# Kernel tuning notes

Measured on AMD Instinct MI355X. Metric: run time of the kernel, lower is better.

The kernel has to match this reference:

```python
import jax, jax.numpy as jnp
import numpy as np

B, S, E, H = 4, 1024, 768, 12
DH = E // H  # per-head dim = 64
PRIOR_VAR = 0.01


def _kl(mu, logvar):
    # kl_regularizer from the source: logvar (units,) broadcasts against mu (in,units)
    t = (jnp.log(PRIOR_VAR) - 1.0 - logvar
         + jnp.log1p(jnp.exp(logvar)) / PRIOR_VAR
         + mu * mu / PRIOR_VAR)
    return 0.5 * jnp.mean(t)


def _linear_first(x, w_mu, w_sigma):
    mu = x @ w_mu
    W_Sigma = jnp.log1p(jnp.exp(w_sigma))            # softplus(w_sigma)
    xs = x / x.shape[-1]                              # x / dim (dim = last dim of x)
    xx = jnp.sum(xs * xs, axis=-1, keepdims=True)     # [B,S,1]
    Sigma = jax.nn.softplus(xx * W_Sigma)             # [B,S,E]
    return mu, Sigma, _kl(w_mu, w_sigma)


def _linear_not_first(mu_in, Sigma_in, w_mu, w_sigma):
    mu = mu_in @ w_mu
    W_Sigma = jnp.log1p(jnp.exp(w_sigma))
    wm = w_mu / jnp.sqrt(jnp.float32(w_mu.shape[0]))  # w_mu / sqrt(in_dim)
    S1 = Sigma_in @ (wm * wm)                         # w^T Sigma_in w
    xs = mu_in / mu_in.shape[-1]
    S2 = jnp.sum(xs * xs, axis=-1, keepdims=True) * W_Sigma
    S3 = jnp.sum(Sigma_in, axis=-1, keepdims=True) * W_Sigma / W_Sigma.shape[-1]
    Sigma = jax.nn.softplus(S1 + S2 + S3)
    return mu, Sigma, _kl(w_mu, w_sigma)


def _heads(x):
    # [B,S,E] -> [B,H,S,DH]
    return x.reshape(B, S, H, DH).transpose(0, 2, 1, 3)


def setup_inputs() -> dict:
    key = jax.random.key(0)
    ks = jax.random.split(key, 9)
    glorot = lambda k: jax.random.normal(k, (E, E), jnp.float32) * jnp.sqrt(2.0 / (E + E))
    sig = lambda k: jax.random.uniform(k, (E,), jnp.float32, minval=-4.6, maxval=-2.25)
    return {
        "x": jax.random.normal(ks[0], (B, S, E), jnp.float32),
        "wq_mu": glorot(ks[1]), "wq_sigma": sig(ks[2]),
        "wk_mu": glorot(ks[3]), "wk_sigma": sig(ks[4]),
        "wv_mu": glorot(ks[5]), "wv_sigma": sig(ks[6]),
        "wo_mu": glorot(ks[7]), "wo_sigma": sig(ks[8]),
    }


def reference(x, wq_mu, wq_sigma, wk_mu, wk_sigma, wv_mu, wv_sigma, wo_mu, wo_sigma):
    # dropout is identity in eval mode (training=False)
    mq, sq, klq = _linear_first(x, wq_mu, wq_sigma)
    mk, sk, klk = _linear_first(x, wk_mu, wk_sigma)
    mv, sv, klv = _linear_first(x, wv_mu, wv_sigma)
    mq, sq, mk, sk, mv, sv = map(_heads, (mq, sq, mk, sk, mv, sv))

    dk = jnp.float32(DH)
    mu_score = jnp.einsum('bhqd,bhkd->bhqk', mq, mk)
    a = jnp.einsum('bhqd,bhkd->bhqk', mq * mq / dk, sk)
    b = jnp.einsum('bhqd,bhkd->bhqk', mk * mk / dk, sq)   # matmul(mk^2/dk, sq^T) as in TF source
    c = jnp.einsum('bhqd,bhkd->bhqk', sq / jnp.sqrt(dk), sk / jnp.sqrt(dk))
    sigma_score = a + b + c

    mu_scaled = mu_score / jnp.sqrt(dk)
    sigma_scaled = sigma_score / dk
    w = jax.nn.softmax(mu_scaled, axis=-1)               # [B,H,S,S]
    wd = jnp.float32(S)
    grad = (w - w * w) ** 2
    Sw = grad * sigma_scaled / wd

    mu_att = jnp.einsum('bhqk,bhkd->bhqd', w, mv)
    d = jnp.einsum('bhqk,bhkd->bhqd', w * w / wd, sv)
    e = jnp.einsum('bhqk,bhkd->bhqd', Sw, mv * mv / wd)
    f = jnp.einsum('bhqk,bhkd->bhqd', Sw / jnp.sqrt(wd), sv / jnp.sqrt(wd))
    sig_att = jax.nn.softplus(d + e + f)

    mu_cat = mu_att.transpose(0, 2, 1, 3).reshape(B, S, E)
    sig_cat = sig_att.transpose(0, 2, 1, 3).reshape(B, S, E)

    mu_out, Sigma_out, klo = _linear_not_first(mu_cat, sig_cat, wo_mu, wo_sigma)
    Sigma_out = jax.nn.softplus(Sigma_out)               # extra softplus in call()
    kl = klq + klk + klv + klo
    return mu_out, Sigma_out, kl
```

## Files before the change

### kernel.cpp

```cpp
#include <hip/hip_runtime.h>
#include <math.h>

#define EN 768
#define SN 1024
#define HN 12
#define BSN 4096
#define BSE 3145728

typedef __attribute__((ext_vector_type(8))) short bf16x8;
typedef __attribute__((ext_vector_type(4))) float f32x4;
typedef __attribute__((ext_vector_type(4))) unsigned short u16x4;
typedef unsigned short u16;

#define OFF_XX   0u
#define OFF_RC   16384u
#define OFF_WSIG 32768u
#define OFF_KL   45056u
#define OFF_ZI   49152u
#define OFF_WT   262144u
#define OFF_QH   4980736u
#define OFF_KH   11272192u
#define OFF_SQD  17563648u
#define OFF_SKD  23855104u
#define OFF_MVT  30146560u
#define OFF_MV2  36438016u
#define OFF_SVT  42729472u
#define OFF_MUH  49020928u
#define OFF_SGH  55312384u

__device__ __forceinline__ float sp_f(float x){
  return fmaxf(x, 0.f) + log1pf(__expf(-fabsf(x)));
}
__device__ __forceinline__ u16 f2b(float f){
  unsigned u = __float_as_uint(f);
  return (u16)((u + 0x7fffu + ((u>>16)&1u)) >> 16);
}
__device__ __forceinline__ float b2f(u16 h){
  return __uint_as_float(((unsigned)h)<<16);
}
__device__ __forceinline__ f32x4 mfma16(bf16x8 a, bf16x8 b, f32x4 c){
  return __builtin_amdgcn_mfma_f32_16x16x32_bf16(a, b, c, 0, 0, 0);
}
__device__ __forceinline__ bf16x8 ldsr(const u16* t, int row, int sg){
  int a16 = (row<<3) + (sg ^ (row&7));
  return *(const bf16x8*)(t + (a16<<3));
}
__device__ __forceinline__ void stage64(u16* dst, const u16* src, int rstride, int tid){
  #pragma unroll
  for (int it=0; it<2; ++it){
    int idx = (it<<8) + tid;
    int row = idx>>3, seg = idx&7;
    bf16x8 v = *(const bf16x8*)(src + (long)row*rstride + (seg<<3));
    int a16 = (row<<3) + (seg ^ (row&7));
    *(bf16x8*)(dst + (a16<<3)) = v;
  }
}

__device__ __forceinline__ float blk_reduce(float v, float* tmp){
  #pragma unroll
  for (int off = 32; off; off >>= 1) v += __shfl_down(v, off, 64);
  int w = threadIdx.x >> 6;
  if ((threadIdx.x & 63) == 0) tmp[w] = v;
  __syncthreads();
  float r = 0.f;
  if (threadIdx.x == 0) r = tmp[0] + tmp[1] + tmp[2] + tmp[3];
  __syncthreads();
  return r;
}

__global__ void k_prep(const float* __restrict__ s0, const float* __restrict__ s1,
                       const float* __restrict__ s2, const float* __restrict__ s3,
                       float* __restrict__ wsig, float* __restrict__ klacc){
  __shared__ float tmp[4];
  const float* src = (blockIdx.x==0)?s0:(blockIdx.x==1)?s1:(blockIdx.x==2)?s2:s3;
  int l = blockIdx.x;
  float ssum=0.f, spsum=0.f;
  for (int j=threadIdx.x; j<EN; j+=256){
    float sg = src[j];
    float w  = log1pf(__expf(sg));
    wsig[l*EN+j] = w;
    ssum += sg; spsum += w;
  }
  float a = blk_reduce(ssum, tmp);
  float b = blk_reduce(spsum, tmp);
  if (threadIdx.x==0){ atomicAdd(&klacc[1], a); atomicAdd(&klacc[2], b); }
}

__global__ void k_xx(const float* __restrict__ x, float* __restrict__ xx){
  __shared__ float tmp[4];
  int r = blockIdx.x;
  const float* xr = x + (long)r*EN;
  float s=0.f;
  for (int j=threadIdx.x; j<EN; j+=256){ float v = xr[j]; s += v*v; }
  float t = blk_reduce(s, tmp);
  if (threadIdx.x==0) xx[r] = t*(1.0f/589824.0f);
}

__global__ void k_mu2(const float* __restrict__ w0, const float* __restrict__ w1,
                      const float* __restrict__ w2, const float* __restrict__ w3,
                      float* __restrict__ klacc){
  __shared__ float tmp[4];
  const float* w = (blockIdx.y==0)?w0:(blockIdx.y==1)?w1:(blockIdx.y==2)?w2:w3;
  const float4* w4 = (const float4*)w;
  float s=0.f;
  for (int i=blockIdx.x*256+threadIdx.x; i<147456; i+=gridDim.x*256){
    float4 v = w4[i];
    s += v.x*v.x + v.y*v.y + v.z*v.z + v.w*v.w;
  }
  float r = blk_reduce(s, tmp);
  if (threadIdx.x==0) atomicAdd(&klacc[0], r);
}

__global__ void k_wt(const float* __restrict__ w0, const float* __restrict__ w1,
                     const float* __restrict__ w2, const float* __restrict__ w3,
                     u16* __restrict__ wt){
  __shared__ float t[64*65];
  const float* W = (blockIdx.z==0)?w0:(blockIdx.z==1)?w1:(blockIdx.z==2)?w2:w3;
  u16* WT = wt + (long)blockIdx.z*589824;
  int r0 = blockIdx.y<<6, c0 = blockIdx.x<<6;
  int tid = threadIdx.x;
  #pragma unroll
  for (int it=0; it<16; ++it){
    int idx=(it<<8)+tid; int r=idx>>6, c=idx&63;
    t[c*65+r] = W[(long)(r0+r)*EN + c0+c];
  }
  __syncthreads();
  #pragma unroll
  for (int it=0; it<16; ++it){
    int idx=(it<<8)+tid; int c=idx>>6, r=idx&63;
    WT[(long)(c0+c)*EN + r0+r] = f2b(t[c*65+r]);
  }
}

__global__ void k_sigarr(const float* __restrict__ xx, const float* __restrict__ wsig,
                         u16* __restrict__ sqd, u16* __restrict__ skd){
  int r = blockIdx.x;
  float xr = xx[r];
  for (int c=threadIdx.x; c<EN; c+=256){
    sqd[(long)r*EN+c] = f2b(sp_f(xr*wsig[c])*(1.0f/64.0f));
    skd[(long)r*EN+c] = f2b(sp_f(xr*wsig[EN+c])*(1.0f/64.0f));
  }
}

__global__ void k_svt(const float* __restrict__ xx, const float* __restrict__ wsig,
                      u16* __restrict__ svT){
  __shared__ float sxx[64], swv[64];
  int kt=blockIdx.x, h=blockIdx.y, b=blockIdx.z, tid=threadIdx.x;
  if (tid < 64){
    sxx[tid] = xx[(long)b*SN + (kt<<6) + tid];
    swv[tid] = wsig[2*EN + (h<<6) + tid];
  }
  __syncthreads();
  long obase = (((long)(b*HN+h))<<6)*SN + (kt<<6);
  #pragma unroll
  for (int it=0; it<16; ++it){
    int idx=(it<<8)+tid; int d=idx>>6, k=idx&63;
    svT[obase + (long)d*SN + k] = f2b(sp_f(sxx[k]*swv[d]));
  }
}

__global__ __launch_bounds__(256)
void k_projmm(const float* __restrict__ x, const u16* __restrict__ WT,
              u16* __restrict__ oq, u16* __restrict__ ok,
              u16* __restrict__ mvT, u16* __restrict__ mv2T){
  __shared__ __align__(16) u16 lds[8192];
  u16* At = lds; u16* Bt = lds + 4096;
  const int tid = threadIdx.x;
  const int w = tid>>6, l = tid&63, l15 = l&15, g = l>>4;
  const int m0 = blockIdx.y<<6, n0 = blockIdx.x<<6;
  const u16* Wt = WT + (long)blockIdx.z*589824;
  f32x4 acc[4];
  #pragma unroll
  for (int t=0;t<4;++t){ acc[t][0]=0;acc[t][1]=0;acc[t][2]=0;acc[t][3]=0; }
  for (int k0=0; k0<EN; k0+=64){
    __syncthreads();
    #pragma unroll
    for (int it=0; it<2; ++it){
      int idx=(it<<8)+tid; int row=idx>>3, seg=idx&7;
      const float* sp = x + (long)(m0+row)*EN + k0 + (seg<<3);
      float4 a = *(const float4*)sp; float4 c = *(const float4*)(sp+4);
      bf16x8 v;
      v[0]=(short)f2b(a.x); v[1]=(short)f2b(a.y); v[2]=(short)f2b(a.z); v[3]=(short)f2b(a.w);
      v[4]=(short)f2b(c.x); v[5]=(short)f2b(c.y); v[6]=(short)f2b(c.z); v[7]=(short)f2b(c.w);
      int a16=(row<<3)+(seg^(row&7));
      *(bf16x8*)(At + (a16<<3)) = v;
    }
    stage64(Bt, Wt + (long)n0*EN + k0, EN, tid);
    __syncthreads();
    #pragma unroll
    for (int s=0;s<2;++s){
      int sg=(s<<2)+g;
      bf16x8 af = ldsr(At, (w<<4)+l15, sg);
      #pragma unroll
      for (int t=0;t<4;++t)
        acc[t] = mfma16(af, ldsr(Bt,(t<<4)+l15,sg), acc[t]);
    }
  }
  if (blockIdx.z < 2){
    u16* out = blockIdx.z ? ok : oq;
    #pragma unroll
    for (int t=0;t<4;++t){
      int col = n0 + (t<<4) + l15;
      #pragma unroll
      for (int r=0;r<4;++r){
        long row = m0 + (w<<4) + (g<<2) + r;
        out[row*EN + col] = f2b(acc[t][r]);
      }
    }
  } else {
    int b  = m0 >> 10;
    int hh = n0 >> 6;
    long obase = (((long)(b*HN+hh))<<6)*SN;
    int tok0 = (m0 & 1023) + (w<<4) + (g<<2);
    #pragma unroll
    for (int t=0;t<4;++t){
      int d = (t<<4) + l15;
      u16x4 m4, s4;
      #pragma unroll
      for (int r=0;r<4;++r){
        u16 mb = f2b(acc[t][r]);
        m4[r] = mb;
        float mf = b2f(mb);
        s4[r] = f2b(mf*mf);
      }
      *(u16x4*)&mvT[obase + (long)d*SN + tok0]  = m4;
      *(u16x4*)&mv2T[obase + (long)d*SN + tok0] = s4;
    }
  }
}

__global__ __launch_bounds__(256)
void k_z(const u16* __restrict__ qh, const u16* __restrict__ kh,
         float* __restrict__ zi){
  __shared__ __align__(16) u16 Tk[4096];
  const int tid = threadIdx.x;
  const int w = tid>>6, l = tid&63, l15 = l&15, g = l>>4;
  const int i = blockIdx.x;
  const int xcd = i & 7, slot = i >> 3;
  const int qt = slot & 15;
  const int pair = xcd*6 + (slot >> 4);
  const int h = pair % HN, b = pair / HN;
  const int q0 = qt<<6;
  const long bS = (long)b*SN;
  bf16x8 amq[2];
  {
    long qrow = (bS + q0 + (w<<4) + l15) * EN;
    #pragma unroll
    for (int s=0;s<2;++s)
      amq[s] = *(const bf16x8*)(qh + qrow + (h<<6) + (s<<5) + (g<<3));
  }
  const u16* khb = kh + bS*EN + (h<<6);
  f32x4 zacc = {0.f,0.f,0.f,0.f};
  for (int kt=0; kt<16; ++kt){
    __syncthreads();
    stage64(Tk, khb + (long)(kt<<6)*EN, EN, tid);
    __syncthreads();
    f32x4 smu[4];
    #pragma unroll
    for (int t=0;t<4;++t){ smu[t][0]=0;smu[t][1]=0;smu[t][2]=0;smu[t][3]=0; }
    #pragma unroll
    for (int s=0;s<2;++s){
      int sg=(s<<2)+g;
      #pragma unroll
      for (int t=0;t<4;++t)
        smu[t] = mfma16(amq[s], ldsr(Tk,(t<<4)+l15,sg), smu[t]);
    }
    #pragma unroll
    for (int t=0;t<4;++t)
      #pragma unroll
      for (int r=0;r<4;++r)
        zacc[r] += __expf(smu[t][r]*0.125f);
  }
  #pragma unroll
  for (int m=1; m<16; m<<=1){
    #pragma unroll
    for (int r=0;r<4;++r) zacc[r] += __shfl_xor(zacc[r], m, 64);
  }
  if (l15 == 0){
    long zbase = (((long)(b*HN+h))<<10) + q0 + (w<<4) + (g<<2);
    #pragma unroll
    for (int r=0;r<4;++r) zi[zbase + r] = 1.0f/zacc[r];
  }
}

__global__ __launch_bounds__(512, 2)
void k_attn(const u16* __restrict__ qh, const u16* __restrict__ kh,
            const u16* __restrict__ sqd, const u16* __restrict__ skd,
            const u16* __restrict__ mvT, const u16* __restrict__ svT,
            const u16* __restrict__ mv2T, const float* __restrict__ zi,
            u16* __restrict__ muh, u16* __restrict__ sgh){
  extern __shared__ u16 lds2[];
  u16* Tk  = lds2;
  u16* Tsk = lds2 + 4096;
  u16* Tsq = lds2 + 8192;
  u16* Tmv = lds2 + 12288;
  u16* Tsv = lds2 + 16384;
  u16* Tm2 = lds2 + 20480;
  const int tid = threadIdx.x;
  const int w = tid>>6, l = tid&63, l15 = l&15, g = l>>4;
  u16* Pw = lds2 + 24576 + (w<<11);
  u16* Pg = Pw + 1024;
  const int i = blockIdx.x;
  const int xcd = i & 7, slot = i >> 3;
  const int qt = slot & 7;
  const int pair = xcd*6 + (slot >> 3);
  const int h = pair % HN, b = pair / HN;
  const int q0 = qt<<7;
  const long bS = (long)b*SN;

  bf16x8 amq[2], acb[2], amk2[2];
  {
    long qrow = (bS + q0 + (w<<4) + l15) * EN;
    #pragma unroll
    for (int s=0;s<2;++s){
      int eoff = (h<<6) + (s<<5) + (g<<3);
      bf16x8 q8 = *(const bf16x8*)(qh + qrow + eoff);
      bf16x8 k8 = *(const bf16x8*)(kh + qrow + eoff);
      bf16x8 s8 = *(const bf16x8*)(sqd + qrow + eoff);
      amq[s] = q8;
      bf16x8 t2, tc;
      #pragma unroll
      for (int j=0;j<8;++j){
        float kv = b2f((u16)k8[j]);
        t2[j] = (short)f2b(kv*kv);
        float qv = b2f((u16)q8[j]);
        float sv = b2f((u16)s8[j]) * 64.0f;
        tc[j] = (short)f2b(qv*qv + sv);
      }
      amk2[s] = t2; acb[s] = tc;
    }
  }
  float zl[4];
  {
    long zbase = (((long)(b*HN+h))<<10) + q0 + (w<<4) + (g<<2);
    #pragma unroll
    for (int r=0;r<4;++r) zl[r] = zi[zbase + r];
  }

  const u16* khb = kh  + bS*EN + (h<<6);
  const u16* skb = skd + bS*EN + (h<<6);
  const u16* sqb = sqd + bS*EN + (h<<6);
  const long hb64 = ((long)(b*HN+h))<<6;
  const u16* mvb = mvT  + hb64*SN;
  const u16* svb = svT  + hb64*SN;
  const u16* m2b = mv2T + hb64*SN;

  f32x4 accM[4], acc2[4], acc3[4];
  #pragma unroll
  for (int t=0;t<4;++t){
    accM[t][0]=0;accM[t][1]=0;accM[t][2]=0;accM[t][3]=0;
    acc2[t][0]=0;acc2[t][1]=0;acc2[t][2]=0;acc2[t][3]=0;
    acc3[t][0]=0;acc3[t][1]=0;acc3[t][2]=0;acc3[t][3]=0;
  }

  const int srow = tid>>3, sseg = tid&7;
  const int a16o = (((srow<<3) + (sseg ^ (srow&7)))<<3);

  for (int kt=0; kt<16; ++kt){
    __syncthreads();
    {
      long off1 = (long)((kt<<6)+srow)*EN + (sseg<<3);
      long off2 = (long)srow*SN + (kt<<6) + (sseg<<3);
      bf16x8 v0 = *(const bf16x8*)(khb+off1);
      bf16x8 v1 = *(const bf16x8*)(skb+off1);
      bf16x8 v2 = *(const bf16x8*)(sqb+off1);
      bf16x8 v3 = *(const bf16x8*)(mvb+off2);
      bf16x8 v4 = *(const bf16x8*)(svb+off2);
      bf16x8 v5 = *(const bf16x8*)(m2b+off2);
      *(bf16x8*)(Tk +a16o) = v0;
      *(bf16x8*)(Tsk+a16o) = v1;
      *(bf16x8*)(Tsq+a16o) = v2;
      *(bf16x8*)(Tmv+a16o) = v3;
      *(bf16x8*)(Tsv+a16o) = v4;
      *(bf16x8*)(Tm2+a16o) = v5;
    }
    __syncthreads();

    #pragma unroll
    for (int t=0;t<4;++t){
      f32x4 smu = {0.f,0.f,0.f,0.f}, ssg = {0.f,0.f,0.f,0.f};
      #pragma unroll
      for (int s=0;s<2;++s){
        int sg=(s<<2)+g;
        int rn = (t<<4)+l15;
        smu = mfma16(amq[s],  ldsr(Tk, rn,sg), smu);
        ssg = mfma16(acb[s],  ldsr(Tsk,rn,sg), ssg);
        ssg = mfma16(amk2[s], ldsr(Tsq,rn,sg), ssg);
      }
      #pragma unroll
      for (int r=0;r<4;++r){
        float e  = __expf(smu[r]*0.125f);
        float wv = e*zl[r];
        float u  = wv - wv*wv;
        float sw = u*u*ssg[r]*(1.0f/65536.0f);
        int prow = (g<<2)+r, pcol = (t<<4)+l15;
        int off = (((prow<<3) + ((pcol>>3) ^ (prow&7)))<<3) + (pcol&7);
        Pw[off] = f2b(wv);
        Pg[off] = f2b(sw);
      }
    }
    asm volatile("s_waitcnt lgkmcnt(0)" ::: "memory");
    #pragma unroll
    for (int s=0;s<2;++s){
      int sg=(s<<2)+g;
      bf16x8 aw = ldsr(Pw, l15, sg);
      bf16x8 ag = ldsr(Pg, l15, sg);
      bf16x8 pa;
      #pragma unroll
      for (int j=0;j<8;++j){
        float wf = b2f((u16)aw[j]);
        pa[j] = (short)f2b(wf*wf + b2f((u16)ag[j]));
      }
      #pragma unroll
      for (int t=0;t<4;++t){
        int rn = (t<<4)+l15;
        accM[t] = mfma16(aw, ldsr(Tmv,rn,sg), accM[t]);
        acc2[t] = mfma16(pa, ldsr(Tsv,rn,sg), acc2[t]);
        acc3[t] = mfma16(ag, ldsr(Tm2,rn,sg), acc3[t]);
      }
    }
  }
  long grow0 = bS + q0 + (w<<4) + (g<<2);
  #pragma unroll
  for (int t=0;t<4;++t){
    int col = (h<<6) + (t<<4) + l15;
    #pragma unroll
    for (int r=0;r<4;++r){
      long o = (grow0 + r)*EN + col;
      muh[o] = f2b(accM[t][r]);
      sgh[o] = f2b(sp_f((acc2[t][r]+acc3[t][r])*(1.0f/1024.0f)));
    }
  }
}

__global__ void k_rows(const u16* __restrict__ muh, const u16* __restrict__ sgh,
                       float* __restrict__ rcomb){
  __shared__ float tmp[4];
  int r = blockIdx.x;
  const u16* m = muh + (long)r*EN;
  const u16* s = sgh + (long)r*EN;
  float s1=0.f, s2=0.f;
  for (int j=threadIdx.x; j<EN; j+=256){ float a=b2f(m[j]); s1+=a*a; s2+=b2f(s[j]); }
  float r1 = blk_reduce(s1, tmp);
  float r2 = blk_reduce(s2, tmp);
  if (threadIdx.x==0) rcomb[r] = r1*(1.0f/589824.0f) + r2*(1.0f/768.0f);
}

__global__ __launch_bounds__(256)
void k_outmm(const u16* __restrict__ muh, const u16* __restrict__ sgh,
             const u16* __restrict__ WTo, const float* __restrict__ rcomb,
             const float* __restrict__ wso, float* __restrict__ mu_out,
             float* __restrict__ sg_out){
  __shared__ __align__(16) u16 lds[12288];
  u16* Am = lds; u16* As = lds + 4096; u16* Bt = lds + 8192;
  const int tid = threadIdx.x;
  const int w = tid>>6, l = tid&63, l15 = l&15, g = l>>4;
  const int m0 = blockIdx.y<<6, n0 = blockIdx.x<<6;
  f32x4 accM[4], accS[4];
  #pragma unroll
  for (int t=0;t<4;++t){
    accM[t][0]=0;accM[t][1]=0;accM[t][2]=0;accM[t][3]=0;
    accS[t][0]=0;accS[t][1]=0;accS[t][2]=0;accS[t][3]=0;
  }
  for (int k0=0; k0<EN; k0+=64){
    __syncthreads();
    stage64(Am, muh + (long)m0*EN + k0, EN, tid);
    stage64(As, sgh + (long)m0*EN + k0, EN, tid);
    stage64(Bt, WTo + (long)n0*EN + k0, EN, tid);
    __syncthreads();
    #pragma unroll
    for (int s=0;s<2;++s){
      int sg=(s<<2)+g;
      bf16x8 am = ldsr(Am, (w<<4)+l15, sg);
      bf16x8 as = ldsr(As, (w<<4)+l15, sg);
      #pragma unroll
      for (int t=0;t<4;++t){
        bf16x8 bw = ldsr(Bt,(t<<4)+l15,sg);
        bf16x8 b2;
        #pragma unroll
        for (int j=0;j<8;++j){ float f=b2f((u16)bw[j]); b2[j]=(short)f2b(f*f); }
        accM[t] = mfma16(am, bw, accM[t]);
        accS[t] = mfma16(as, b2, accS[t]);
      }
    }
  }
  float rc4[4];
  #pragma unroll
  for (int r=0;r<4;++r) rc4[r] = rcomb[m0 + (w<<4) + (g<<2) + r];
  #pragma unroll
  for (int t=0;t<4;++t){
    int col = n0 + (t<<4) + l15;
    float wsc = wso[col];
    #pragma unroll
    for (int r=0;r<4;++r){
      long row = m0 + (w<<4) + (g<<2) + r;
      mu_out[row*EN + col] = accM[t][r];
      float spre = accS[t][r]*(1.0f/768.0f) + rc4[r]*wsc;
      sg_out[row*EN + col] = sp_f(sp_f(spre));
    }
  }
}

__global__ void k_klf(const float* __restrict__ klacc, float* __restrict__ out){
  float Smu2 = klacc[0], Ssig = klacc[1], Ssp = klacc[2];
  const float C = -5.60517018599f;
  out[0] = 0.5f*(4.f*C - Ssig*(1.0f/768.0f) + Ssp*(1.0f/7.68f) + Smu2*(1.0f/5898.24f));
}

extern "C" void kernel_launch(void* const* d_in, const int* in_sizes, int n_in,
                              void* d_out, int out_size, void* d_ws, size_t ws_size,
                              hipStream_t stream) {
  (void)in_sizes; (void)n_in; (void)out_size; (void)ws_size;
  const float* x      = (const float*)d_in[0];
  const float* wq_mu  = (const float*)d_in[1];
  const float* wq_sig = (const float*)d_in[2];
  const float* wk_mu  = (const float*)d_in[3];
  const float* wk_sig = (const float*)d_in[4];
  const float* wv_mu  = (const float*)d_in[5];
  const float* wv_sig = (const float*)d_in[6];
  const float* wo_mu  = (const float*)d_in[7];
  const float* wo_sig = (const float*)d_in[8];

  char* wsb = (char*)d_ws;
  float* xx    = (float*)(wsb + OFF_XX);
  float* rc    = (float*)(wsb + OFF_RC);
  float* wsig  = (float*)(wsb + OFF_WSIG);
  float* kla   = (float*)(wsb + OFF_KL);
  float* zi    = (float*)(wsb + OFF_ZI);
  u16*   WT    = (u16*)(wsb + OFF_WT);
  u16*   qh    = (u16*)(wsb + OFF_QH);
  u16*   kh    = (u16*)(wsb + OFF_KH);
  u16*   sqd   = (u16*)(wsb + OFF_SQD);
  u16*   skd   = (u16*)(wsb + OFF_SKD);
  u16*   mvT   = (u16*)(wsb + OFF_MVT);
  u16*   mv2T  = (u16*)(wsb + OFF_MV2);
  u16*   svT   = (u16*)(wsb + OFF_SVT);
  u16*   muh   = (u16*)(wsb + OFF_MUH);
  u16*   sgh   = (u16*)(wsb + OFF_SGH);

  float* mu_out = (float*)d_out;
  float* sg_out = mu_out + BSE;
  float* kl_out = mu_out + 2*BSE;

  (void)hipMemsetAsync(kla, 0, 3*sizeof(float), stream);
  k_prep<<<4, 256, 0, stream>>>(wq_sig, wk_sig, wv_sig, wo_sig, wsig, kla);
  k_xx<<<BSN, 256, 0, stream>>>(x, xx);
  k_mu2<<<dim3(64,4), 256, 0, stream>>>(wq_mu, wk_mu, wv_mu, wo_mu, kla);
  k_wt<<<dim3(12,12,4), 256, 0, stream>>>(wq_mu, wk_mu, wv_mu, wo_mu, WT);
  k_sigarr<<<BSN, 256, 0, stream>>>(xx, wsig, sqd, skd);
  k_svt<<<dim3(16,HN,4), 256, 0, stream>>>(xx, wsig, svT);
  k_projmm<<<dim3(12,64,3), 256, 0, stream>>>(x, WT, qh, kh, mvT, mv2T);
  k_z<<<768, 256, 0, stream>>>(qh, kh, zi);

  const int attn_lds = 40960*2;
  (void)hipFuncSetAttribute((const void*)k_attn,
                      hipFuncAttributeMaxDynamicSharedMemorySize, attn_lds);
  k_attn<<<384, 512, attn_lds, stream>>>(qh, kh, sqd, skd, mvT, svT,
                                         mv2T, zi, muh, sgh);
  k_rows<<<BSN, 256, 0, stream>>>(muh, sgh, rc);
  k_outmm<<<dim3(12,64), 256, 0, stream>>>(muh, sgh, WT + 3l*589824, rc,
                                           wsig + 3*EN, mu_out, sg_out);
  k_klf<<<1, 1, 0, stream>>>(kla, kl_out);
}
```

Baseline: 378.3 us.

## Register-prefetch next K/V tiles, pack P tiles, use hardware bf16 convert

In k_attn and k_z, the next key-tile loads are issued into registers right after the LDS barrier, so global latency overlaps the MFMA work of the current tile. k_z moves to 512-thread blocks covering 128 queries each, with half as many blocks. The attention P/G probability tiles are interleaved into one 32-bit LDS array written with v_cvt_pk_bf16_f32, and the squared-weight conversions in k_attn and k_outmm use the packed hardware convert instead of software rounding. Holding the prefetched tiles raises register pressure, and the rounding mode of the hardware convert may differ slightly from the manual f2b.

```diff
diff --git a/kernel.cpp b/kernel.cpp
--- a/kernel.cpp
+++ b/kernel.cpp
@@ -10,6 +10,7 @@
 typedef __attribute__((ext_vector_type(8))) short bf16x8;
 typedef __attribute__((ext_vector_type(4))) float f32x4;
 typedef __attribute__((ext_vector_type(4))) unsigned short u16x4;
+typedef __attribute__((ext_vector_type(4))) unsigned int u32x4;
 typedef unsigned short u16;
 
 #define OFF_XX   0u
@@ -38,8 +39,28 @@
 __device__ __forceinline__ float b2f(u16 h){
   return __uint_as_float(((unsigned)h)<<16);
 }
+__device__ __forceinline__ unsigned cvtpk(float lo, float hi){
+  unsigned r;
+  asm("v_cvt_pk_bf16_f32 %0, %1, %2" : "=v"(r) : "v"(lo), "v"(hi));
+  return r;
+}
+__device__ __forceinline__ bf16x8 u2b(u32x4 v){
+  union{u32x4 u; bf16x8 b;} x; x.u = v; return x.b;
+}
 __device__ __forceinline__ f32x4 mfma16(bf16x8 a, bf16x8 b, f32x4 c){
   return __builtin_amdgcn_mfma_f32_16x16x32_bf16(a, b, c, 0, 0, 0);
+}
+__device__ __forceinline__ bf16x8 sq8(bf16x8 a){
+  union{bf16x8 b; u32x4 u;} x; x.b = a;
+  u32x4 r;
+  #pragma unroll
+  for (int i=0;i<4;++i){
+    unsigned v = x.u[i];
+    float f0 = __uint_as_float(v<<16);
+    float f1 = __uint_as_float(v & 0xffff0000u);
+    r[i] = cvtpk(f0*f0, f1*f1);
+  }
+  return u2b(r);
 }
 __device__ __forceinline__ bf16x8 ldsr(const u16* t, int row, int sg){
   int a16 = (row<<3) + (sg ^ (row&7));
@@ -229,7 +250,7 @@
   }
 }
 
-__global__ __launch_bounds__(256)
+__global__ __launch_bounds__(512)
 void k_z(const u16* __restrict__ qh, const u16* __restrict__ kh,
          float* __restrict__ zi){
   __shared__ __align__(16) u16 Tk[4096];
@@ -237,10 +258,10 @@
   const int w = tid>>6, l = tid&63, l15 = l&15, g = l>>4;
   const int i = blockIdx.x;
   const int xcd = i & 7, slot = i >> 3;
-  const int qt = slot & 15;
-  const int pair = xcd*6 + (slot >> 4);
+  const int qt = slot & 7;
+  const int pair = xcd*6 + (slot >> 3);
   const int h = pair % HN, b = pair / HN;
-  const int q0 = qt<<6;
+  const int q0 = qt<<7;
   const long bS = (long)b*SN;
   bf16x8 amq[2];
   {
@@ -250,11 +271,16 @@
       amq[s] = *(const bf16x8*)(qh + qrow + (h<<6) + (s<<5) + (g<<3));
   }
   const u16* khb = kh + bS*EN + (h<<6);
+  const int srow = tid>>3, sseg = tid&7;
+  const int a16o = (((srow<<3) + (sseg ^ (srow&7)))<<3);
+  bf16x8 pf = *(const bf16x8*)(khb + (long)srow*EN + (sseg<<3));
   f32x4 zacc = {0.f,0.f,0.f,0.f};
   for (int kt=0; kt<16; ++kt){
     __syncthreads();
-    stage64(Tk, khb + (long)(kt<<6)*EN, EN, tid);
-    __syncthreads();
+    *(bf16x8*)(Tk + a16o) = pf;
+    __syncthreads();
+    if (kt < 15)
+      pf = *(const bf16x8*)(khb + (long)(((kt+1)<<6)+srow)*EN + (sseg<<3));
     f32x4 smu[4];
     #pragma unroll
     for (int t=0;t<4;++t){ smu[t][0]=0;smu[t][1]=0;smu[t][2]=0;smu[t][3]=0; }
@@ -298,8 +324,7 @@
   u16* Tm2 = lds2 + 20480;
   const int tid = threadIdx.x;
   const int w = tid>>6, l = tid&63, l15 = l&15, g = l>>4;
-  u16* Pw = lds2 + 24576 + (w<<11);
-  u16* Pg = Pw + 1024;
+  unsigned* Pu = (unsigned*)(lds2 + 24576) + (w<<10);
   const int i = blockIdx.x;
   const int xcd = i & 7, slot = i >> 3;
   const int qt = slot & 7;
@@ -356,25 +381,37 @@
   const int srow = tid>>3, sseg = tid&7;
   const int a16o = (((srow<<3) + (sseg ^ (srow&7)))<<3);
 
+  bf16x8 pf0, pf1, pf2, pf3, pf4, pf5;
+  {
+    long off1 = (long)srow*EN + (sseg<<3);
+    long off2 = (long)srow*SN + (sseg<<3);
+    pf0 = *(const bf16x8*)(khb+off1);
+    pf1 = *(const bf16x8*)(skb+off1);
+    pf2 = *(const bf16x8*)(sqb+off1);
+    pf3 = *(const bf16x8*)(mvb+off2);
+    pf4 = *(const bf16x8*)(svb+off2);
+    pf5 = *(const bf16x8*)(m2b+off2);
+  }
+
   for (int kt=0; kt<16; ++kt){
     __syncthreads();
-    {
-      long off1 = (long)((kt<<6)+srow)*EN + (sseg<<3);
-      long off2 = (long)srow*SN + (kt<<6) + (sseg<<3);
-      bf16x8 v0 = *(const bf16x8*)(khb+off1);
-      bf16x8 v1 = *(const bf16x8*)(skb+off1);
-      bf16x8 v2 = *(const bf16x8*)(sqb+off1);
-      bf16x8 v3 = *(const bf16x8*)(mvb+off2);
-      bf16x8 v4 = *(const bf16x8*)(svb+off2);
-      bf16x8 v5 = *(const bf16x8*)(m2b+off2);
-      *(bf16x8*)(Tk +a16o) = v0;
-      *(bf16x8*)(Tsk+a16o) = v1;
-      *(bf16x8*)(Tsq+a16o) = v2;
-      *(bf16x8*)(Tmv+a16o) = v3;
-      *(bf16x8*)(Tsv+a16o) = v4;
-      *(bf16x8*)(Tm2+a16o) = v5;
-    }
-    __syncthreads();
+    *(bf16x8*)(Tk +a16o) = pf0;
+    *(bf16x8*)(Tsk+a16o) = pf1;
+    *(bf16x8*)(Tsq+a16o) = pf2;
+    *(bf16x8*)(Tmv+a16o) = pf3;
+    *(bf16x8*)(Tsv+a16o) = pf4;
+    *(bf16x8*)(Tm2+a16o) = pf5;
+    __syncthreads();
+    if (kt < 15){
+      long off1 = (long)(((kt+1)<<6)+srow)*EN + (sseg<<3);
+      long off2 = (long)srow*SN + ((kt+1)<<6) + (sseg<<3);
+      pf0 = *(const bf16x8*)(khb+off1);
+      pf1 = *(const bf16x8*)(skb+off1);
+      pf2 = *(const bf16x8*)(sqb+off1);
+      pf3 = *(const bf16x8*)(mvb+off2);
+      pf4 = *(const bf16x8*)(svb+off2);
+      pf5 = *(const bf16x8*)(m2b+off2);
+    }
 
     #pragma unroll
     for (int t=0;t<4;++t){
@@ -394,23 +431,28 @@
         float u  = wv - wv*wv;
         float sw = u*u*ssg[r]*(1.0f/65536.0f);
         int prow = (g<<2)+r, pcol = (t<<4)+l15;
-        int off = (((prow<<3) + ((pcol>>3) ^ (prow&7)))<<3) + (pcol&7);
-        Pw[off] = f2b(wv);
-        Pg[off] = f2b(sw);
+        int a32 = (((prow<<3) + ((pcol>>3)^(prow&7)))<<3) + (pcol&7);
+        Pu[a32] = cvtpk(wv, sw);
       }
     }
     asm volatile("s_waitcnt lgkmcnt(0)" ::: "memory");
     #pragma unroll
     for (int s=0;s<2;++s){
       int sg=(s<<2)+g;
-      bf16x8 aw = ldsr(Pw, l15, sg);
-      bf16x8 ag = ldsr(Pg, l15, sg);
-      bf16x8 pa;
-      #pragma unroll
-      for (int j=0;j<8;++j){
-        float wf = b2f((u16)aw[j]);
-        pa[j] = (short)f2b(wf*wf + b2f((u16)ag[j]));
-      }
+      const u32x4* pp = (const u32x4*)(Pu + (((l15<<3) + (sg ^ (l15&7)))<<3));
+      u32x4 pA = pp[0], pB = pp[1];
+      unsigned qa[8] = {pA[0],pA[1],pA[2],pA[3],pB[0],pB[1],pB[2],pB[3]};
+      u32x4 awu, agu, pau;
+      #pragma unroll
+      for (int i2=0;i2<4;++i2){
+        unsigned lo = qa[2*i2], hi = qa[2*i2+1];
+        awu[i2] = (lo & 0xffffu) | (hi << 16);
+        agu[i2] = (lo >> 16) | (hi & 0xffff0000u);
+        float w0 = __uint_as_float(lo<<16), g0 = __uint_as_float(lo & 0xffff0000u);
+        float w1 = __uint_as_float(hi<<16), g1 = __uint_as_float(hi & 0xffff0000u);
+        pau[i2] = cvtpk(fmaf(w0,w0,g0), fmaf(w1,w1,g1));
+      }
+      bf16x8 aw = u2b(awu), ag = u2b(agu), pa = u2b(pau);
       #pragma unroll
       for (int t=0;t<4;++t){
         int rn = (t<<4)+l15;
@@ -476,11 +518,8 @@
       #pragma unroll
       for (int t=0;t<4;++t){
         bf16x8 bw = ldsr(Bt,(t<<4)+l15,sg);
-        bf16x8 b2;
-        #pragma unroll
-        for (int j=0;j<8;++j){ float f=b2f((u16)bw[j]); b2[j]=(short)f2b(f*f); }
         accM[t] = mfma16(am, bw, accM[t]);
-        accS[t] = mfma16(as, b2, accS[t]);
+        accS[t] = mfma16(as, sq8(bw), accS[t]);
       }
     }
   }
@@ -550,7 +589,7 @@
   k_sigarr<<<BSN, 256, 0, stream>>>(xx, wsig, sqd, skd);
   k_svt<<<dim3(16,HN,4), 256, 0, stream>>>(xx, wsig, svT);
   k_projmm<<<dim3(12,64,3), 256, 0, stream>>>(x, WT, qh, kh, mvT, mv2T);
-  k_z<<<768, 256, 0, stream>>>(qh, kh, zi);
+  k_z<<<384, 512, 0, stream>>>(qh, kh, zi);
 
   const int attn_lds = 40960*2;
   (void)hipFuncSetAttribute((const void*)k_attn,
```

Measured after the change: 359.2 us. 5.1% less time.
